# Optimization experiments

Measured on AMD Instinct MI355X. Metric: run time of the kernel, lower is better.

Reference implementation:

```python
import jax, jax.numpy as jnp
import numpy as np

B, N, H = 8, 2048, 1024

def setup_inputs() -> dict:
    key = jax.random.key(0)
    ks = jax.random.split(key, 10)
    s = 1.0 / np.sqrt(2 * H)
    return {
        "sem": jax.random.normal(ks[0], (B, N, H), jnp.float32),
        "temp": jax.random.normal(ks[1], (B, N, H), jnp.float32),
        "Wq": jax.random.normal(ks[2], (2 * H, H), jnp.float32) * s,
        "bq": jnp.zeros((H,), jnp.float32),
        "Wk": jax.random.normal(ks[3], (2 * H, H), jnp.float32) * s,
        "bk": jnp.zeros((H,), jnp.float32),
        "Wv": jax.random.normal(ks[4], (2 * H, H), jnp.float32) * s,
        "bv": jnp.zeros((H,), jnp.float32),
        "Wg": jax.random.normal(ks[5], (2 * H, 1), jnp.float32) * s,
        "bg": jnp.zeros((1,), jnp.float32),
    }

def reference(sem, temp, Wq, bq, Wk, bk, Wv, bv, Wg, bg):
    combined = jnp.concatenate([sem, temp], axis=-1)          # [B,N,2H]
    Q = combined @ Wq + bq                                    # [B,N,H]
    K = combined @ Wk + bk
    V = combined @ Wv + bv
    scale = 1.0 / jnp.sqrt(jnp.asarray(Q.shape[-1], Q.dtype))
    scores = jnp.einsum('bqh,bkh->bqk', Q, K) * scale         # [B,N,N]
    attn = jax.nn.softmax(scores, axis=-1)
    gate = jax.nn.sigmoid(combined @ Wg + bg)                 # [B,N,1]
    attn_weights = attn * gate                                # row-wise gate
    fused = jnp.einsum('bqk,bkh->bqh', attn_weights, V)       # [B,N,H]
    return fused + sem, attn_weights.mean(axis=1)             # [B,N,H], [B,N]
```

## Files before the change

### kernel.cpp

```cpp
#include <hip/hip_runtime.h>
#include <stdint.h>
#include <math.h>

#define NB 8
#define NN 2048
#define HH 1024
#define K2 2048
#define MM 16384

typedef unsigned short u16;
typedef __attribute__((ext_vector_type(8))) short short8v;
typedef __attribute__((ext_vector_type(4))) float floatx4;

__device__ __forceinline__ float bf2f(u16 u) { return __uint_as_float(((unsigned)u) << 16); }
__device__ __forceinline__ u16 f2bf(float f) {
  unsigned u = __float_as_uint(f);
  unsigned r = (u + 0x7fffu + ((u >> 16) & 1u)) >> 16;
  return (u16)r;
}

__device__ __forceinline__ void async16(const void* g, void* lds) {
  __builtin_amdgcn_global_load_lds((const __attribute__((address_space(1))) void*)g,
                                   (__attribute__((address_space(3))) void*)lds,
                                   16, 0, 0);
}

__device__ __forceinline__ int xcd_swz(int bid, int nblk) {
  return (bid & 7) * (nblk >> 3) + (bid >> 3);
}

__device__ __forceinline__ void gemm256_core(const u16* __restrict__ A, int lda,
                                             const u16* __restrict__ Bt, int ldb,
                                             int rowA0, int rowB0, int K,
                                             u16* sA, u16* sB, floatx4 acc[8][4]) {
  const int t = threadIdx.x;
  const int w = t >> 6, l = t & 63;
  const int wr = w >> 2, wc = w & 3;

#pragma unroll
  for (int mi = 0; mi < 8; mi++)
#pragma unroll
    for (int ni = 0; ni < 4; ni++) { floatx4 z = {0.f,0.f,0.f,0.f}; acc[mi][ni] = z; }

  const int cS = ((t & 3) ^ ((t >> 3) & 3)) << 3;
  const u16* gA0 = A + (size_t)(rowA0 + (t >> 2)) * lda + cS;
  const u16* gA1 = A + (size_t)(rowA0 + 128 + (t >> 2)) * lda + cS;
  const u16* gB0 = Bt + (size_t)(rowB0 + (t >> 2)) * ldb + cS;
  const u16* gB1 = Bt + (size_t)(rowB0 + 128 + (t >> 2)) * ldb + cS;
  char* dA = (char*)sA + (w << 10) + (l << 4);
  char* dB = (char*)sB + (w << 10) + (l << 4);

  const int fr = l & 15;
  const int xr = (fr >> 1) & 3;
  const int ch = ((l >> 4) ^ xr) << 4;
  const int abase = (wr * 128 + fr) * 64 + ch;
  const int bbase = (wc * 64 + fr) * 64 + ch;

  const int NTt = K >> 5;

#define STG(bi, kt) { const int ko_ = (kt) << 5;                       \
    char* dA_ = dA + (bi) * 16384; char* dB_ = dB + (bi) * 16384;      \
    async16(gA0 + ko_, dA_);        async16(gA1 + ko_, dA_ + 8192);    \
    async16(gB0 + ko_, dB_);        async16(gB1 + ko_, dB_ + 8192); }

  STG(0, 0);
  STG(1, 1);

  int bc = 0, bs = 2;
  for (int tt = 0; tt < NTt; ++tt) {
    if (tt < NTt - 1) { asm volatile("s_waitcnt vmcnt(4)" ::: "memory"); }
    else              { asm volatile("s_waitcnt vmcnt(0)" ::: "memory"); }
    __builtin_amdgcn_s_barrier();
    if (tt + 2 < NTt) STG(bs, tt + 2);

    const char* a = (const char*)sA + bc * 16384;
    const char* b = (const char*)sB + bc * 16384;
    short8v bfr[4], afr[8];
#pragma unroll
    for (int ni = 0; ni < 4; ni++) bfr[ni] = *(const short8v*)(b + bbase + ni * 1024);
#pragma unroll
    for (int mi = 0; mi < 8; mi++) afr[mi] = *(const short8v*)(a + abase + mi * 1024);
    __builtin_amdgcn_s_setprio(1);
#pragma unroll
    for (int mi = 0; mi < 8; mi++)
#pragma unroll
      for (int ni = 0; ni < 4; ni++)
        acc[mi][ni] = __builtin_amdgcn_mfma_f32_16x16x32_bf16(afr[mi], bfr[ni], acc[mi][ni], 0, 0, 0);
    __builtin_amdgcn_s_setprio(0);
    bc = (bc == 2) ? 0 : bc + 1;
    bs = (bs == 2) ? 0 : bs + 1;
  }
#undef STG
}

__global__ void __launch_bounds__(256) k_prep_x(const float* __restrict__ sem,
                                                const float* __restrict__ temp,
                                                u16* __restrict__ X) {
  size_t i = (((size_t)blockIdx.x * 256) + threadIdx.x) << 2;
  int row = (int)(i >> 11);
  int col = (int)(i & 2047);
  const float* src = (col < 1024) ? (sem + (size_t)row * 1024 + col)
                                  : (temp + (size_t)row * 1024 + (col - 1024));
  float4 v = *(const float4*)src;
  ushort4 o;
  o.x = f2bf(v.x); o.y = f2bf(v.y); o.z = f2bf(v.z); o.w = f2bf(v.w);
  *(ushort4*)(X + i) = o;
}

__global__ void __launch_bounds__(256) k_transpose_w(const float* __restrict__ W,
                                                     u16* __restrict__ Wt) {
  __shared__ float s[32][33];
  int tile = blockIdx.x;
  int nt = tile & 31, kt = tile >> 5;
  int tx = threadIdx.x & 31, ty = threadIdx.x >> 5;
  int n0 = nt << 5, k0 = kt << 5;
#pragma unroll
  for (int j = 0; j < 32; j += 8)
    s[ty + j][tx] = W[(size_t)(k0 + ty + j) * 1024 + (n0 + tx)];
  __syncthreads();
#pragma unroll
  for (int j = 0; j < 32; j += 8)
    Wt[(size_t)(n0 + ty + j) * 2048 + (k0 + tx)] = f2bf(s[tx][ty + j]);
}

__global__ void __launch_bounds__(512, 2) k_proj_qkv(const u16* __restrict__ X,
                                                     const u16* __restrict__ Wt,
                                                     const float* __restrict__ bq,
                                                     const float* __restrict__ bk,
                                                     const float* __restrict__ bv,
                                                     u16* __restrict__ Qb,
                                                     u16* __restrict__ Kb,
                                                     u16* __restrict__ Vt) {
  __shared__ __align__(16) u16 sA[3 * 8192];
  __shared__ __align__(16) u16 sB[3 * 8192];
  int tile = xcd_swz(blockIdx.x, 768);
  int bm = tile / 12, bn = tile - bm * 12;
  floatx4 acc[8][4];
  gemm256_core(X, K2, Wt, K2, bm * 256, bn * 256, K2, sA, sB, acc);

  const int t = threadIdx.x, w = t >> 6, l = t & 63;
  const int wr = w >> 2, wc = w & 3;
  const int r0 = bm * 256 + wr * 128 + ((l >> 4) << 2);
  const int cg0 = bn * 256 + wc * 64 + (l & 15);
  const int which = bn >> 2;
  const float* bias = which == 0 ? bq : which == 1 ? bk : bv;
#pragma unroll
  for (int ni = 0; ni < 4; ni++) {
    int c1 = (cg0 + ni * 16) & 1023;
    float bvv = bias[c1];
#pragma unroll
    for (int mi = 0; mi < 8; mi++)
#pragma unroll
      for (int i = 0; i < 4; i++) {
        int rg = r0 + mi * 16 + i;
        u16 ob = f2bf(acc[mi][ni][i] + bvv);
        if (which == 0)      Qb[(size_t)rg * 1024 + c1] = ob;
        else if (which == 1) Kb[(size_t)rg * 1024 + c1] = ob;
        else                 Vt[((size_t)(rg >> 11) * 1024 + c1) * 2048 + (rg & 2047)] = ob;
      }
  }
}

__global__ void __launch_bounds__(256) k_gate(const u16* __restrict__ X, const float* __restrict__ Wg,
                                              const float* __restrict__ bg, float* __restrict__ gate) {
  int row = blockIdx.x * 4 + (threadIdx.x >> 6);
  int l = threadIdx.x & 63;
  const short* xr = (const short*)(X + (size_t)row * 2048);
  float s = 0.f;
#pragma unroll
  for (int i = 0; i < 4; i++) {
    int k = i * 512 + l * 8;
    short8v v = *(const short8v*)&xr[k];
#pragma unroll
    for (int j = 0; j < 8; j++) s += bf2f((u16)v[j]) * Wg[k + j];
  }
#pragma unroll
  for (int off = 32; off > 0; off >>= 1) s += __shfl_xor(s, off);
  if (l == 0) gate[row] = 1.f / (1.f + expf(-(s + bg[0])));
}

__global__ void __launch_bounds__(512, 2) k_scores(const u16* __restrict__ Q, const u16* __restrict__ Kb,
                                                   u16* __restrict__ E, float* __restrict__ lsum) {
  __shared__ __align__(16) u16 sA[3 * 8192];
  __shared__ __align__(16) u16 sB[3 * 8192];
  int tile = xcd_swz(blockIdx.x, 512);
  int b = tile >> 6, r = tile & 63, bm = r >> 3, bn = r & 7;
  const u16* A = Q + (size_t)b * NN * HH;
  const u16* Bt = Kb + (size_t)b * NN * HH;
  floatx4 acc[8][4];
  gemm256_core(A, HH, Bt, HH, bm * 256, bn * 256, HH, sA, sB, acc);

  u16* Eb = E + (size_t)b * NN * NN;
  float* lb = lsum + b * NN;
  const int t = threadIdx.x, w = t >> 6, l = t & 63;
  const int wr = w >> 2, wc = w & 3;
  const int q0 = bm * 256 + wr * 128 + ((l >> 4) << 2);
  const int k0c = bn * 256 + wc * 64 + (l & 15);
#pragma unroll
  for (int mi = 0; mi < 8; mi++)
#pragma unroll
    for (int i = 0; i < 4; i++) {
      int q = q0 + mi * 16 + i;
      float rs = 0.f;
#pragma unroll
      for (int ni = 0; ni < 4; ni++) {
        float e = expf(acc[mi][ni][i] * 0.03125f);
        Eb[(size_t)q * NN + k0c + ni * 16] = f2bf(e);
        rs += e;
      }
      rs += __shfl_xor(rs, 1);
      rs += __shfl_xor(rs, 2);
      rs += __shfl_xor(rs, 4);
      rs += __shfl_xor(rs, 8);
      if ((l & 15) == 0) atomicAdd(&lb[q], rs);
    }
}

__global__ void __launch_bounds__(512, 2) k_pv(const u16* __restrict__ E, const u16* __restrict__ Vt,
                                               const float* __restrict__ gate, const float* __restrict__ lsum,
                                               const float* __restrict__ sem, float* __restrict__ out) {
  __shared__ __align__(16) u16 sA[3 * 8192];
  __shared__ __align__(16) u16 sB[3 * 8192];
  int tile = xcd_swz(blockIdx.x, 256);
  int b = tile >> 5, r = tile & 31, bm = r >> 2, bn = r & 3;
  const u16* A = E + (size_t)b * NN * NN;
  const u16* Bt = Vt + (size_t)b * HH * NN;
  floatx4 acc[8][4];
  gemm256_core(A, NN, Bt, NN, bm * 256, bn * 256, NN, sA, sB, acc);

  const int t = threadIdx.x, w = t >> 6, l = t & 63;
  const int wr = w >> 2, wc = w & 3;
  const int q0 = bm * 256 + wr * 128 + ((l >> 4) << 2);
  const int h0 = bn * 256 + wc * 64 + (l & 15);
#pragma unroll
  for (int mi = 0; mi < 8; mi++)
#pragma unroll
    for (int i = 0; i < 4; i++) {
      int q = q0 + mi * 16 + i;
      size_t gq = (size_t)b * NN + q;
      float wq = gate[gq] / lsum[gq];
#pragma unroll
      for (int ni = 0; ni < 4; ni++) {
        int h = h0 + ni * 16;
        out[gq * HH + h] = acc[mi][ni][i] * wq + sem[gq * HH + h];
      }
    }
}

__global__ void __launch_bounds__(256) k_colmean(const u16* __restrict__ E, const float* __restrict__ gate,
                                                 const float* __restrict__ lsum, float* __restrict__ cm) {
  __shared__ float wsh[256];
  int bid = blockIdx.x;
  int b = bid >> 6, rest = bid & 63;
  int ks = rest >> 3, qc = rest & 7;
  int t = threadIdx.x;
  {
    size_t gq = (size_t)b * NN + qc * 256 + t;
    wsh[t] = gate[gq] / lsum[gq];
  }
  __syncthreads();
  int k = ks * 256 + t;
  const u16* Eb = E + ((size_t)b * NN + (size_t)qc * 256) * NN + k;
  float s = 0.f;
  for (int q = 0; q < 256; q++) s += wsh[q] * bf2f(Eb[(size_t)q * NN]);
  atomicAdd(&cm[b * NN + k], s * (1.f / 2048.f));
}

extern "C" void kernel_launch(void* const* d_in, const int* in_sizes, int n_in,
                              void* d_out, int out_size, void* d_ws, size_t ws_size,
                              hipStream_t stream) {
  const float* sem  = (const float*)d_in[0];
  const float* temp = (const float*)d_in[1];
  const float* Wq   = (const float*)d_in[2];
  const float* bq   = (const float*)d_in[3];
  const float* Wk   = (const float*)d_in[4];
  const float* bk   = (const float*)d_in[5];
  const float* Wv   = (const float*)d_in[6];
  const float* bv   = (const float*)d_in[7];
  const float* Wg   = (const float*)d_in[8];
  const float* bg   = (const float*)d_in[9];
  float* out = (float*)d_out;

  char* ws = (char*)d_ws;
  u16* X      = (u16*)ws;
  u16* E      = X;
  u16* WqkvT  = (u16*)(ws + 67108864);
  u16* Qb     = (u16*)(ws + 79691776);
  u16* Kb     = (u16*)(ws + 113246208);
  u16* Vt     = (u16*)(ws + 146800640);
  float* gate = (float*)(ws + 180355072);
  float* lsum = (float*)(ws + 180420608);

  hipMemsetAsync(lsum, 0, 65536, stream);
  hipMemsetAsync(out + 16777216, 0, 65536, stream);

  k_prep_x<<<32768, 256, 0, stream>>>(sem, temp, X);
  k_transpose_w<<<2048, 256, 0, stream>>>(Wq, WqkvT);
  k_transpose_w<<<2048, 256, 0, stream>>>(Wk, WqkvT + (size_t)1024 * 2048);
  k_transpose_w<<<2048, 256, 0, stream>>>(Wv, WqkvT + (size_t)2048 * 2048);
  k_proj_qkv<<<768, 512, 0, stream>>>(X, WqkvT, bq, bk, bv, Qb, Kb, Vt);
  k_gate<<<4096, 256, 0, stream>>>(X, Wg, bg, gate);
  k_scores<<<512, 512, 0, stream>>>(Qb, Kb, E, lsum);
  k_pv<<<256, 512, 0, stream>>>(E, Vt, gate, lsum, sem, out);
  k_colmean<<<512, 256, 0, stream>>>(E, gate, lsum, out + 16777216);
}
```

Before: 580.4 us.

## Split GEMM k-step into two phases interleaving A/B staging with MFMA halves

Restructures the GEMM main loop into two half-phases: each loads half the A fragments, issues the async global-to-LDS staging for A (then B) of a future tile, and runs half the MFMAs, with barriers and explicit lgkmcnt waits between phases. The goal is to interleave memory issue with MFMA work and reduce register pressure from holding all eight A fragments. In exchange it adds more barriers per iteration, which can add synchronization stalls.

New measurement: 580.2 us. Within noise of the previous version (-0.0%).

```diff
diff --git a/kernel.cpp b/kernel.cpp
--- a/kernel.cpp
+++ b/kernel.cpp
@@ -51,46 +51,69 @@
   char* dB = (char*)sB + (w << 10) + (l << 4);
 
   const int fr = l & 15;
-  const int xr = (fr >> 1) & 3;
-  const int ch = ((l >> 4) ^ xr) << 4;
+  const int ch = (((l >> 4) ^ ((fr >> 1) & 3)) << 4);
   const int abase = (wr * 128 + fr) * 64 + ch;
   const int bbase = (wc * 64 + fr) * 64 + ch;
 
-  const int NTt = K >> 5;
-
-#define STG(bi, kt) { const int ko_ = (kt) << 5;                       \
-    char* dA_ = dA + (bi) * 16384; char* dB_ = dB + (bi) * 16384;      \
-    async16(gA0 + ko_, dA_);        async16(gA1 + ko_, dA_ + 8192);    \
-    async16(gB0 + ko_, dB_);        async16(gB1 + ko_, dB_ + 8192); }
-
-  STG(0, 0);
-  STG(1, 1);
+  const int NT = K >> 5;
+
+#define STGA(bi, kt) { const int ko_ = (kt) << 5; char* d_ = dA + (bi) * 16384; \
+    async16(gA0 + ko_, d_); async16(gA1 + ko_, d_ + 8192); }
+#define STGB(bi, kt) { const int ko_ = (kt) << 5; char* d_ = dB + (bi) * 16384; \
+    async16(gB0 + ko_, d_); async16(gB1 + ko_, d_ + 8192); }
+
+  STGA(0, 0); STGB(0, 0);
+  STGA(1, 1); STGB(1, 1);
+  asm volatile("s_waitcnt vmcnt(4)" ::: "memory");
+  __builtin_amdgcn_s_barrier();
 
   int bc = 0, bs = 2;
-  for (int tt = 0; tt < NTt; ++tt) {
-    if (tt < NTt - 1) { asm volatile("s_waitcnt vmcnt(4)" ::: "memory"); }
-    else              { asm volatile("s_waitcnt vmcnt(0)" ::: "memory"); }
-    __builtin_amdgcn_s_barrier();
-    if (tt + 2 < NTt) STG(bs, tt + 2);
-
+  for (int tt = 0; tt < NT; ++tt) {
     const char* a = (const char*)sA + bc * 16384;
     const char* b = (const char*)sB + bc * 16384;
-    short8v bfr[4], afr[8];
+    const bool stg = (tt + 2 < NT);
+
+    short8v bfr[4], afr[4];
 #pragma unroll
     for (int ni = 0; ni < 4; ni++) bfr[ni] = *(const short8v*)(b + bbase + ni * 1024);
 #pragma unroll
-    for (int mi = 0; mi < 8; mi++) afr[mi] = *(const short8v*)(a + abase + mi * 1024);
+    for (int mi = 0; mi < 4; mi++) afr[mi] = *(const short8v*)(a + abase + mi * 1024);
+    if (stg) STGA(bs, tt + 2);
+    __builtin_amdgcn_s_barrier();
+    asm volatile("s_waitcnt lgkmcnt(0)" ::: "memory");
     __builtin_amdgcn_s_setprio(1);
 #pragma unroll
-    for (int mi = 0; mi < 8; mi++)
+    for (int mi = 0; mi < 4; mi++)
 #pragma unroll
       for (int ni = 0; ni < 4; ni++)
         acc[mi][ni] = __builtin_amdgcn_mfma_f32_16x16x32_bf16(afr[mi], bfr[ni], acc[mi][ni], 0, 0, 0);
     __builtin_amdgcn_s_setprio(0);
+    __builtin_amdgcn_s_barrier();
+
+    short8v afr2[4];
+#pragma unroll
+    for (int mi = 0; mi < 4; mi++) afr2[mi] = *(const short8v*)(a + abase + (4 + mi) * 1024);
+    if (stg) STGB(bs, tt + 2);
+    __builtin_amdgcn_s_barrier();
+    asm volatile("s_waitcnt lgkmcnt(0)" ::: "memory");
+    __builtin_amdgcn_s_setprio(1);
+#pragma unroll
+    for (int mi = 0; mi < 4; mi++)
+#pragma unroll
+      for (int ni = 0; ni < 4; ni++)
+        acc[4 + mi][ni] = __builtin_amdgcn_mfma_f32_16x16x32_bf16(afr2[mi], bfr[ni], acc[4 + mi][ni], 0, 0, 0);
+    __builtin_amdgcn_s_setprio(0);
+    if (tt < NT - 1) {
+      if (stg) { asm volatile("s_waitcnt vmcnt(4)" ::: "memory"); }
+      else     { asm volatile("s_waitcnt vmcnt(0)" ::: "memory"); }
+    }
+    __builtin_amdgcn_s_barrier();
+
     bc = (bc == 2) ? 0 : bc + 1;
     bs = (bs == 2) ? 0 : bs + 1;
   }
-#undef STG
+#undef STGA
+#undef STGB
 }
 
 __global__ void __launch_bounds__(256) k_prep_x(const float* __restrict__ sem,
```
